# Kernel tuning notes

Hardware: AMD Instinct MI355X
Metric: run time of the kernel (lower is better)

Reference implementation:

```python
import jax, jax.numpy as jnp
import numpy as np

DEPTH = 4
NUM_HEADS = 8
SCALE = 0.25  # (128/8)**-0.5


def _ln(x, g, b):
    m = x.mean(-1, keepdims=True)
    v = ((x - m) ** 2).mean(-1, keepdims=True)
    return (x - m) / jnp.sqrt(v + 1e-5) * g + b


def _mlp_stack(x, params):
    # AsymFormer's MLP default activation is identity, so pure linear stack
    for w, b in params:
        x = x @ w + b
    return x


def _forward(joint_in, relation_in, conn,
             je_w1, je_b1, je_w2, je_b2, je_w3, je_b3,
             re_w1, re_b1, re_w2, re_b2, re_w3, re_b3,
             qkv_w, qkv_b, rconv_w, rconv_b, proj_w, proj_b,
             ln1_g, ln1_b, ln2_g, ln2_b, ln3_g, ln3_b,
             mw1, mb1, mw2, mb2, ng, nb,
             dw1, db1, dw2, db2, dw3, db3):
    jf = _mlp_stack(joint_in, [(je_w1, je_b1), (je_w2, je_b2), (je_w3, je_b3)])
    rf = _mlp_stack(relation_in, [(re_w1, re_b1), (re_w2, re_b2), (re_w3, re_b3)])  # (B,N,N,C)
    B, N, C = jf.shape
    H = NUM_HEADS
    HS = C // H
    for i in range(DEPTH):
        x = _ln(jf, ln1_g[i], ln1_b[i])
        r = _ln(rf, ln2_g[i], ln2_b[i])
        qkv = (x @ qkv_w[i] + qkv_b[i]).reshape(B, N, 3, H, HS)
        q = qkv[:, :, 0].transpose(0, 2, 1, 3)  # (B,H,N,HS)
        k = qkv[:, :, 1].transpose(0, 2, 1, 3)
        v = qkv[:, :, 2].transpose(0, 2, 1, 3)
        attn_J = jnp.einsum('bhnd,bhmd->bhnm', q, k)
        attn_R = (r @ rconv_w[i] + rconv_b[i]).transpose(0, 3, 1, 2)  # (B,H,N,N)
        attn = (attn_J + attn_R) * conn[:, None, :, :] * SCALE
        attn = jax.nn.softmax(attn, axis=-1)
        o = jnp.einsum('bhnm,bhmd->bhnd', attn, v).transpose(0, 2, 1, 3).reshape(B, N, C)
        jf = jf + (o @ proj_w[i] + proj_b[i])
        h = _ln(jf, ln3_g[i], ln3_b[i])
        h = jax.nn.gelu(h @ mw1[i] + mb1[i], approximate=False) @ mw2[i] + mb2[i]
        jf = jf + h
    jf = _ln(jf, ng, nb)
    return _mlp_stack(jf, [(dw1, db1), (dw2, db2), (dw3, db3)])


def setup_inputs() -> dict:
    key = jax.random.key(0)
    ks = iter(jax.random.split(key, 64))
    B, N, C, H, Dp = 8, 256, 128, 8, DEPTH

    def rn(shape, s=0.02):
        return jax.random.normal(next(ks), shape, jnp.float32) * s

    inp = {}
    inp['joint_in'] = jax.random.normal(next(ks), (B, N, 96), jnp.float32)
    inp['relation_in'] = jax.random.normal(next(ks), (B, N, N, 26), jnp.float32)
    inp['conn'] = jax.random.uniform(next(ks), (B, N, N), jnp.float32)
    # joint encoder 96->256->256->128
    for j, (di, do) in enumerate([(96, 256), (256, 256), (256, 128)]):
        inp[f'je_w{j+1}'] = rn((di, do)); inp[f'je_b{j+1}'] = jnp.zeros((do,), jnp.float32)
    # relation encoder 26->256->256->128
    for j, (di, do) in enumerate([(26, 256), (256, 256), (256, 128)]):
        inp[f're_w{j+1}'] = rn((di, do)); inp[f're_b{j+1}'] = jnp.zeros((do,), jnp.float32)
    # per-block params (stacked over depth)
    inp['qkv_w'] = rn((Dp, C, 3 * C)); inp['qkv_b'] = jnp.zeros((Dp, 3 * C), jnp.float32)
    inp['rconv_w'] = rn((Dp, C, H)); inp['rconv_b'] = jnp.zeros((Dp, H), jnp.float32)
    inp['proj_w'] = rn((Dp, C, C)); inp['proj_b'] = jnp.zeros((Dp, C), jnp.float32)
    for nm in ['ln1', 'ln2', 'ln3']:
        inp[f'{nm}_g'] = jnp.ones((Dp, C), jnp.float32)
        inp[f'{nm}_b'] = jnp.zeros((Dp, C), jnp.float32)
    inp['mw1'] = rn((Dp, C, C)); inp['mb1'] = jnp.zeros((Dp, C), jnp.float32)
    inp['mw2'] = rn((Dp, C, C)); inp['mb2'] = jnp.zeros((Dp, C), jnp.float32)
    inp['ng'] = jnp.ones((C,), jnp.float32); inp['nb'] = jnp.zeros((C,), jnp.float32)
    # decoder 128->256->512->90
    for j, (di, do) in enumerate([(128, 256), (256, 512), (512, 90)]):
        inp[f'dw{j+1}'] = rn((di, do)); inp[f'db{j+1}'] = jnp.zeros((do,), jnp.float32)
    return inp


def reference(joint_in, relation_in, conn,
              je_w1, je_b1, je_w2, je_b2, je_w3, je_b3,
              re_w1, re_b1, re_w2, re_b2, re_w3, re_b3,
              qkv_w, qkv_b, rconv_w, rconv_b, proj_w, proj_b,
              ln1_g, ln1_b, ln2_g, ln2_b, ln3_g, ln3_b,
              mw1, mb1, mw2, mb2, ng, nb,
              dw1, db1, dw2, db2, dw3, db3):
    return _forward(joint_in, relation_in, conn,
                    je_w1, je_b1, je_w2, je_b2, je_w3, je_b3,
                    re_w1, re_b1, re_w2, re_b2, re_w3, re_b3,
                    qkv_w, qkv_b, rconv_w, rconv_b, proj_w, proj_b,
                    ln1_g, ln1_b, ln2_g, ln2_b, ln3_g, ln3_b,
                    mw1, mb1, mw2, mb2, ng, nb,
                    dw1, db1, dw2, db2, dw3, db3)
```

## Files before the change

kernel.cpp:

```cpp
#include <hip/hip_runtime.h>
#include <hip/hip_bf16.h>
#include <math.h>

typedef __hip_bfloat16 bf16;
typedef __attribute__((ext_vector_type(8))) short short8;
typedef __attribute__((ext_vector_type(4))) short s16x4;
typedef __attribute__((ext_vector_type(4))) float f32x4;
typedef __attribute__((ext_vector_type(2))) float f32x2;

#define Bb 8
#define Nn 256
#define Hh 8
#define DEPTHd 4
#define BN 2048
#define RTOT 524288
#define RELB 8192
#define JB 32
#define XTS 136
#define X3S 136

__device__ inline float toF(float v) { return v; }
__device__ inline float toF(bf16 v) { return __bfloat162float(v); }
__device__ inline void stF(float* p, float v) { *p = v; }
__device__ inline void stF(bf16* p, float v) { *p = __float2bfloat16(v); }

__global__ __launch_bounds__(256) void k_relF(
    const float* __restrict__ rin, const bf16* __restrict__ W123t,
    const float* __restrict__ b123, const bf16* __restrict__ gWt,
    const float* __restrict__ sgW, const float* __restrict__ bconst,
    bf16* __restrict__ attnR, const float* __restrict__ jin,
    const bf16* __restrict__ Wj123t, const float* __restrict__ bj123,
    float* __restrict__ jf) {
  __shared__ __align__(16) char smem[17920];
  bf16* x3 = (bf16*)smem;
  float* sstatF = (float*)(smem + 17408);

  const int t = threadIdx.x;
  const int lane = t & 63, wv = t >> 6;
  const int lrow = lane & 15, quad = lane >> 4;
  const bool rel = blockIdx.x < RELB;

  if (!rel) {
    const long r0j = (long)(blockIdx.x - RELB) * 64;
    const long gj = r0j + wv * 16 + lrow;
    short8 aj[3];
#pragma unroll
    for (int ks = 0; ks < 3; ++ks) {
      const float* ap = &jin[gj * 96 + ks * 32 + quad * 8];
      f32x4 f0 = *(const f32x4*)ap;
      f32x4 f1 = *(const f32x4*)(ap + 4);
      bf16 pk[8];
#pragma unroll
      for (int u = 0; u < 4; ++u) {
        pk[u] = __float2bfloat16(f0[u]);
        pk[u + 4] = __float2bfloat16(f1[u]);
      }
      aj[ks] = *(short8*)pk;
    }
#pragma unroll
    for (int cb = 0; cb < 4; ++cb)
#pragma unroll
      for (int ct = 0; ct < 2; ++ct) {
        int colb = cb * 32 + ct * 16;
        f32x4 x = {0.f, 0.f, 0.f, 0.f};
#pragma unroll
        for (int ks = 0; ks < 3; ++ks) {
          short8 bw = *(const short8*)&Wj123t[(colb + lrow) * 96 + ks * 32 + quad * 8];
          x = __builtin_amdgcn_mfma_f32_16x16x32_bf16(bw, aj[ks], x, 0, 0, 0);
        }
        f32x4 bq = *(const f32x4*)&bj123[colb + quad * 4];
        f32x4 out;
#pragma unroll
        for (int r = 0; r < 4; ++r) out[r] = x[r] + bq[r];
        *(f32x4*)&jf[gj * 128 + colb + quad * 4] = out;
      }
    return;
  }

  short8 a0;
  {
    const long gr = (long)blockIdx.x * 64 + wv * 16 + lrow;
    const float* ap = &rin[gr * 26];
    float v[8];
    if (quad < 3) {
#pragma unroll
      for (int u = 0; u < 4; ++u) {
        f32x2 f = *(const f32x2*)(ap + quad * 8 + u * 2);
        v[u * 2] = f[0];
        v[u * 2 + 1] = f[1];
      }
    } else {
      f32x2 f = *(const f32x2*)(ap + 24);
      v[0] = f[0];
      v[1] = f[1];
#pragma unroll
      for (int u = 2; u < 8; ++u) v[u] = 0.f;
    }
    bf16 pk[8];
#pragma unroll
    for (int u = 0; u < 8; ++u) pk[u] = __float2bfloat16(v[u]);
    a0 = *(short8*)pk;
  }

  float s1 = 0.f, s2 = 0.f;
#pragma unroll
  for (int cb = 0; cb < 4; ++cb)
#pragma unroll
    for (int ct = 0; ct < 2; ++ct) {
      int colb = cb * 32 + ct * 16;
      f32x4 x = {0.f, 0.f, 0.f, 0.f};
      short8 bw = *(const short8*)&W123t[(colb + lrow) * 32 + quad * 8];
      x = __builtin_amdgcn_mfma_f32_16x16x32_bf16(bw, a0, x, 0, 0, 0);
      f32x4 bq = *(const f32x4*)&b123[colb + quad * 4];
      bf16 pk[4];
#pragma unroll
      for (int r = 0; r < 4; ++r) {
        float v = x[r] + bq[r];
        pk[r] = __float2bfloat16(v);
        s1 += v;
        s2 += v * v;
      }
      *(s16x4*)&x3[(wv * 16 + lrow) * X3S + colb + quad * 4] = *(s16x4*)pk;
    }
  s1 += __shfl_xor(s1, 16, 64);
  s2 += __shfl_xor(s2, 16, 64);
  s1 += __shfl_xor(s1, 32, 64);
  s2 += __shfl_xor(s2, 32, 64);
  if (quad == 0) {
    int row = wv * 16 + lrow;
    float mu = s1 * (1.f / 128.f);
    float var = s2 * (1.f / 128.f) - mu * mu;
    sstatF[row * 2] = mu;
    sstatF[row * 2 + 1] = rsqrtf(var + 1e-5f);
  }
  short8 aw0[4], aw1[4];
#pragma unroll
  for (int kk = 0; kk < 4; ++kk) {
    aw0[kk] = *(const short8*)&gWt[lrow * 128 + kk * 32 + quad * 8];
    aw1[kk] = *(const short8*)&gWt[(16 + lrow) * 128 + kk * 32 + quad * 8];
  }
  __syncthreads();

  {
    f32x4 ac0 = {0.f, 0.f, 0.f, 0.f}, ac1 = {0.f, 0.f, 0.f, 0.f};
#pragma unroll
    for (int kk = 0; kk < 4; ++kk) {
      short8 bbx = *(const short8*)&x3[(wv * 16 + lrow) * X3S + kk * 32 + quad * 8];
      ac0 = __builtin_amdgcn_mfma_f32_16x16x32_bf16(aw0[kk], bbx, ac0, 0, 0, 0);
      ac1 = __builtin_amdgcn_mfma_f32_16x16x32_bf16(aw1[kk], bbx, ac1, 0, 0, 0);
    }
    const long r0 = (long)blockIdx.x * 64;
    int drow = wv * 16 + lrow;
    long gr = r0 + drow;
    float mu = sstatF[drow * 2], inv = sstatF[drow * 2 + 1];
    int bb_ = (int)(gr >> 16);
    int nn = (int)((gr >> 8) & 255);
    int mm = (int)(gr & 255);
#pragma unroll
    for (int mt = 0; mt < 2; ++mt) {
      f32x4 a = mt ? ac1 : ac0;
#pragma unroll
      for (int reg = 0; reg < 4; ++reg) {
        int col = mt * 16 + quad * 4 + reg;
        float v = inv * (a[reg] - mu * sgW[col]) + bconst[col];
        int dd = col >> 3, hh = col & 7;
        attnR[((((long)dd * Bb + bb_) * Hh + hh) * Nn + nn) * Nn + mm] =
            __float2bfloat16(v);
      }
    }
  }
}

__global__ void k_prep0(const float* re_w1, const float* re_w2, const float* re_b1,
                        const float* re_b2, const float* je_w1, const float* je_w2,
                        const float* je_b1, const float* je_b2, const float* dw2,
                        const float* dw3, const float* db1, const float* ln2_g,
                        const float* ln2_b, const float* rconv_w, const float* rconv_b,
                        const float* qkv_w, const float* proj_w, const float* mw1,
                        const float* mw2, float* F, float* bT, float* Fj, float* bTj,
                        float* G, float* u1, bf16* gWt, float* sgW, float* bconst,
                        bf16* Wq, bf16* Wp, bf16* Wm1, bf16* Wm2) {
  const int stride = gridDim.x * blockDim.x;
  const int tid = blockIdx.x * blockDim.x + threadIdx.x;
  for (int i = tid; i < 26 * 256; i += stride) {
    int k = i >> 8, d = i & 255;
    float v = 0.f;
    for (int c = 0; c < 256; ++c) v += re_w1[k * 256 + c] * re_w2[c * 256 + d];
    F[i] = v;
  }
  for (int i = tid; i < 256; i += stride) {
    float v = 0.f;
    for (int c = 0; c < 256; ++c) v += re_b1[c] * re_w2[c * 256 + i];
    bT[i] = v + re_b2[i];
  }
  for (int i = tid; i < 96 * 256; i += stride) {
    int k = i >> 8, d = i & 255;
    float v = 0.f;
    for (int c = 0; c < 256; ++c) v += je_w1[k * 256 + c] * je_w2[c * 256 + d];
    Fj[i] = v;
  }
  for (int i = tid; i < 256; i += stride) {
    float v = 0.f;
    for (int c = 0; c < 256; ++c) v += je_b1[c] * je_w2[c * 256 + i];
    bTj[i] = v + je_b2[i];
  }
  for (int i = tid; i < 256 * 90; i += stride) {
    int c = i / 90, m = i - c * 90;
    float v = 0.f;
    for (int d = 0; d < 512; ++d) v += dw2[c * 512 + d] * dw3[d * 90 + m];
    G[i] = v;
  }
  for (int i = tid; i < 512; i += stride) {
    float v = 0.f;
    for (int c = 0; c < 256; ++c) v += db1[c] * dw2[c * 512 + i];
    u1[i] = v;
  }
  for (int i = tid; i < 32 * 128; i += stride) {
    int col = i >> 7, c = i & 127;
    int dd = col >> 3, h = col & 7;
    gWt[i] = __float2bfloat16(ln2_g[dd * 128 + c] * rconv_w[(dd * 128 + c) * 8 + h]);
  }
  if (tid < 32) {
    int dd = tid >> 3, h = tid & 7;
    float sg = 0.f, bc = 0.f;
    for (int c = 0; c < 128; ++c) {
      float w = rconv_w[(dd * 128 + c) * 8 + h];
      sg += ln2_g[dd * 128 + c] * w;
      bc += ln2_b[dd * 128 + c] * w;
    }
    sgW[tid] = sg;
    bconst[tid] = bc + rconv_b[tid];
  }
  for (int i = tid; i < 4 * 384 * 128; i += stride) {
    int d = i / 49152, rem = i - d * 49152;
    int n = rem >> 7, k = rem & 127;
    Wq[i] = __float2bfloat16(qkv_w[d * 49152 + k * 384 + n]);
  }
  for (int i = tid; i < 4 * 128 * 128; i += stride) {
    int d = i >> 14, rem = i & 16383;
    int n = rem >> 7, k = rem & 127;
    Wp[i] = __float2bfloat16(proj_w[d * 16384 + k * 128 + n]);
    Wm1[i] = __float2bfloat16(mw1[d * 16384 + k * 128 + n]);
    Wm2[i] = __float2bfloat16(mw2[d * 16384 + k * 128 + n]);
  }
}

__global__ void k_prep1(const float* F, const float* bT, const float* re_w3,
                        const float* re_b3, const float* Fj, const float* bTj,
                        const float* je_w3, const float* je_b3, const float* dw1,
                        const float* G, const float* u1, const float* db2,
                        const float* dw3, const float* db3, bf16* W123t, float* b123,
                        bf16* Wj123t, float* bj123, bf16* Wd123t, float* bd123p) {
  const int stride = gridDim.x * blockDim.x;
  const int tid = blockIdx.x * blockDim.x + threadIdx.x;
  for (int i = tid; i < 128 * 32; i += stride) {
    int m = i >> 5, k = i & 31;
    float v = 0.f;
    if (k < 26)
      for (int d = 0; d < 256; ++d) v += F[k * 256 + d] * re_w3[d * 128 + m];
    W123t[i] = __float2bfloat16(v);
  }
  for (int i = tid; i < 128; i += stride) {
    float v = 0.f;
    for (int d = 0; d < 256; ++d) v += bT[d] * re_w3[d * 128 + i];
    b123[i] = v + re_b3[i];
  }
  for (int i = tid; i < 128 * 96; i += stride) {
    int m = i / 96, k = i - m * 96;
    float v = 0.f;
    for (int d = 0; d < 256; ++d) v += Fj[k * 256 + d] * je_w3[d * 128 + m];
    Wj123t[i] = __float2bfloat16(v);
  }
  for (int i = tid; i < 128; i += stride) {
    float v = 0.f;
    for (int d = 0; d < 256; ++d) v += bTj[d] * je_w3[d * 128 + i];
    bj123[i] = v + je_b3[i];
  }
  for (int i = tid; i < 128 * 128; i += stride) {
    int m = i >> 7, k = i & 127;
    float v = 0.f;
    if (m < 90)
      for (int c = 0; c < 256; ++c) v += dw1[k * 256 + c] * G[c * 90 + m];
    Wd123t[i] = __float2bfloat16(v);
  }
  for (int i = tid; i < 128; i += stride) {
    float v = 0.f;
    if (i < 90) {
      for (int d = 0; d < 512; ++d) v += (u1[d] + db2[d]) * dw3[d * 90 + i];
      v += db3[i];
    }
    bd123p[i] = v;
  }
}

template <typename TC>
__global__ __launch_bounds__(256) void k_lnqkv(
    const float* __restrict__ A, const float* __restrict__ g,
    const float* __restrict__ b, const bf16* __restrict__ Bt,
    const float* __restrict__ bias, TC* __restrict__ C, int ldc, int ncols) {
  __shared__ __align__(16) bf16 sX[32 * XTS];
  const int t = threadIdx.x;
  const int lane = t & 63;
  const int wv = t >> 6;
  const int lrow = lane & 15, quad = lane >> 4;
  const long row0 = (long)blockIdx.y * 32;
  const int n0 = blockIdx.x * 128;

  {
    int row = t >> 3, prt = t & 7;
    const float* ap = &A[(row0 + row) * 128 + prt * 16];
    float v[16];
    float s1 = 0.f, s2 = 0.f;
#pragma unroll
    for (int u = 0; u < 4; ++u) {
      f32x4 q = *(const f32x4*)(ap + u * 4);
#pragma unroll
      for (int e = 0; e < 4; ++e) {
        v[u * 4 + e] = q[e];
        s1 += q[e];
        s2 += q[e] * q[e];
      }
    }
    s1 += __shfl_xor(s1, 1, 64);
    s2 += __shfl_xor(s2, 1, 64);
    s1 += __shfl_xor(s1, 2, 64);
    s2 += __shfl_xor(s2, 2, 64);
    s1 += __shfl_xor(s1, 4, 64);
    s2 += __shfl_xor(s2, 4, 64);
    float mu = s1 * (1.f / 128.f);
    float inv = rsqrtf(s2 * (1.f / 128.f) - mu * mu + 1e-5f);
#pragma unroll
    for (int u4 = 0; u4 < 4; ++u4) {
      bf16 pk[4];
#pragma unroll
      for (int e = 0; e < 4; ++e) {
        int c = prt * 16 + u4 * 4 + e;
        pk[e] = __float2bfloat16((v[u4 * 4 + e] - mu) * inv * g[c] + b[c]);
      }
      *(s16x4*)&sX[row * XTS + prt * 16 + u4 * 4] = *(s16x4*)pk;
    }
  }
  __syncthreads();

  f32x4 acc[2][2];
#pragma unroll
  for (int i = 0; i < 2; ++i)
#pragma unroll
    for (int j = 0; j < 2; ++j) {
      f32x4 z = {0.f, 0.f, 0.f, 0.f};
      acc[i][j] = z;
    }
#pragma unroll
  for (int k0 = 0; k0 < 128; k0 += 32) {
    short8 af[2], bfr[2];
#pragma unroll
    for (int j = 0; j < 2; ++j)
      bfr[j] = *(const short8*)&Bt[(long)(n0 + wv * 32 + j * 16 + lrow) * 128 + k0 +
                                   quad * 8];
#pragma unroll
    for (int i = 0; i < 2; ++i)
      af[i] = *(const short8*)&sX[(i * 16 + lrow) * XTS + k0 + quad * 8];
#pragma unroll
    for (int i = 0; i < 2; ++i)
#pragma unroll
      for (int j = 0; j < 2; ++j)
        acc[i][j] =
            __builtin_amdgcn_mfma_f32_16x16x32_bf16(af[i], bfr[j], acc[i][j], 0, 0, 0);
  }
#pragma unroll
  for (int i = 0; i < 2; ++i) {
#pragma unroll
    for (int r = 0; r < 4; ++r) {
      long gr = row0 + i * 16 + quad * 4 + r;
#pragma unroll
      for (int j = 0; j < 2; ++j) {
        int gc = n0 + wv * 32 + j * 16 + lrow;
        if (gc < ncols) stF(&C[gr * (long)ldc + gc], acc[i][j][r] + bias[gc]);
      }
    }
  }
}

template <bool QKV>
__global__ __launch_bounds__(256) void k_tailq(
    const bf16* __restrict__ obuf, float* __restrict__ jf, const bf16* __restrict__ Wp,
    const float* __restrict__ pb, const float* __restrict__ g3,
    const float* __restrict__ b3, const bf16* __restrict__ Wm1,
    const float* __restrict__ m1b, const bf16* __restrict__ Wm2,
    const float* __restrict__ m2b, const float* __restrict__ g1n,
    const float* __restrict__ b1n, const bf16* __restrict__ Wqn,
    const float* __restrict__ qbn, float* __restrict__ qkvb) {
  __shared__ __align__(16) bf16 sX[16 * XTS];
  __shared__ __align__(16) bf16 sH[16 * XTS];
  __shared__ float sstat[16][4][2];
  __shared__ float sstatF[16][2];

  const int t = threadIdx.x;
  const int lane = t & 63;
  const int wv = t >> 6;
  const int lrow = lane & 15, quad = lane >> 4;
  const long row0 = (long)blockIdx.x * 16;

  {
    int r = t >> 4, c8 = (t & 15) * 8;
    *(uint4*)&sX[r * XTS + c8] = *(const uint4*)&obuf[(row0 + r) * 128 + c8];
  }
  __syncthreads();

  f32x4 acc[2];
  {
    f32x4 z = {0.f, 0.f, 0.f, 0.f};
    acc[0] = z;
    acc[1] = z;
  }
#pragma unroll
  for (int k0 = 0; k0 < 128; k0 += 32) {
    short8 af = *(const short8*)&sX[lrow * XTS + k0 + quad * 8];
    short8 bfr[2];
#pragma unroll
    for (int j = 0; j < 2; ++j)
      bfr[j] = *(const short8*)&Wp[(wv * 32 + j * 16 + lrow) * 128 + k0 + quad * 8];
#pragma unroll
    for (int j = 0; j < 2; ++j)
      acc[j] = __builtin_amdgcn_mfma_f32_16x16x32_bf16(af, bfr[j], acc[j], 0, 0, 0);
  }
#pragma unroll
  for (int r = 0; r < 4; ++r) {
    int rl = quad * 4 + r;
    long gr = row0 + rl;
    float s1 = 0.f, s2 = 0.f;
#pragma unroll
    for (int j = 0; j < 2; ++j) {
      int gc = wv * 32 + j * 16 + lrow;
      float v = acc[j][r] + pb[gc] + jf[gr * 128 + gc];
      acc[j][r] = v;
      jf[gr * 128 + gc] = v;
      s1 += v;
      s2 += v * v;
    }
#pragma unroll
    for (int m = 1; m < 16; m <<= 1) {
      s1 += __shfl_xor(s1, m, 64);
      s2 += __shfl_xor(s2, m, 64);
    }
    if (lrow == 0) {
      sstat[rl][wv][0] = s1;
      sstat[rl][wv][1] = s2;
    }
  }
  __syncthreads();
  if (t < 16) {
    float s1 = 0.f, s2 = 0.f;
#pragma unroll
    for (int w = 0; w < 4; ++w) {
      s1 += sstat[t][w][0];
      s2 += sstat[t][w][1];
    }
    float mu = s1 * (1.f / 128.f);
    float var = s2 * (1.f / 128.f) - mu * mu;
    sstatF[t][0] = mu;
    sstatF[t][1] = rsqrtf(var + 1e-5f);
  }
  __syncthreads();
#pragma unroll
  for (int r = 0; r < 4; ++r) {
    int rl = quad * 4 + r;
    float mu = sstatF[rl][0], inv = sstatF[rl][1];
#pragma unroll
    for (int j = 0; j < 2; ++j) {
      int gc = wv * 32 + j * 16 + lrow;
      sX[rl * XTS + gc] = __float2bfloat16((acc[j][r] - mu) * inv * g3[gc] + b3[gc]);
    }
  }
  __syncthreads();

  f32x4 acc2[2];
  {
    f32x4 z = {0.f, 0.f, 0.f, 0.f};
    acc2[0] = z;
    acc2[1] = z;
  }
#pragma unroll
  for (int k0 = 0; k0 < 128; k0 += 32) {
    short8 af = *(const short8*)&sX[lrow * XTS + k0 + quad * 8];
    short8 bfr[2];
#pragma unroll
    for (int j = 0; j < 2; ++j)
      bfr[j] = *(const short8*)&Wm1[(wv * 32 + j * 16 + lrow) * 128 + k0 + quad * 8];
#pragma unroll
    for (int j = 0; j < 2; ++j)
      acc2[j] = __builtin_amdgcn_mfma_f32_16x16x32_bf16(af, bfr[j], acc2[j], 0, 0, 0);
  }
#pragma unroll
  for (int r = 0; r < 4; ++r) {
    int rl = quad * 4 + r;
#pragma unroll
    for (int j = 0; j < 2; ++j) {
      int gc = wv * 32 + j * 16 + lrow;
      float v = acc2[j][r] + m1b[gc];
      v = 0.5f * v * (1.f + erff(v * 0.70710678118654752f));
      sH[rl * XTS + gc] = __float2bfloat16(v);
    }
  }
  __syncthreads();

  f32x4 acc3[2];
  {
    f32x4 z = {0.f, 0.f, 0.f, 0.f};
    acc3[0] = z;
    acc3[1] = z;
  }
#pragma unroll
  for (int k0 = 0; k0 < 128; k0 += 32) {
    short8 af = *(const short8*)&sH[lrow * XTS + k0 + quad * 8];
    short8 bfr[2];
#pragma unroll
    for (int j = 0; j < 2; ++j)
      bfr[j] = *(const short8*)&Wm2[(wv * 32 + j * 16 + lrow) * 128 + k0 + quad * 8];
#pragma unroll
    for (int j = 0; j < 2; ++j)
      acc3[j] = __builtin_amdgcn_mfma_f32_16x16x32_bf16(af, bfr[j], acc3[j], 0, 0, 0);
  }
#pragma unroll
  for (int r = 0; r < 4; ++r) {
    int rl = quad * 4 + r;
    long gr = row0 + rl;
    float s1 = 0.f, s2 = 0.f;
#pragma unroll
    for (int j = 0; j < 2; ++j) {
      int gc = wv * 32 + j * 16 + lrow;
      float v = acc3[j][r] + m2b[gc] + jf[gr * 128 + gc];
      acc3[j][r] = v;
      jf[gr * 128 + gc] = v;
      if (QKV) {
        s1 += v;
        s2 += v * v;
      }
    }
    if (QKV) {
#pragma unroll
      for (int m = 1; m < 16; m <<= 1) {
        s1 += __shfl_xor(s1, m, 64);
        s2 += __shfl_xor(s2, m, 64);
      }
      if (lrow == 0) {
        sstat[rl][wv][0] = s1;
        sstat[rl][wv][1] = s2;
      }
    }
  }
  if (!QKV) return;
  __syncthreads();
  if (t < 16) {
    float s1 = 0.f, s2 = 0.f;
#pragma unroll
    for (int w = 0; w < 4; ++w) {
      s1 += sstat[t][w][0];
      s2 += sstat[t][w][1];
    }
    float mu = s1 * (1.f / 128.f);
    float var = s2 * (1.f / 128.f) - mu * mu;
    sstatF[t][0] = mu;
    sstatF[t][1] = rsqrtf(var + 1e-5f);
  }
  __syncthreads();
#pragma unroll
  for (int r = 0; r < 4; ++r) {
    int rl = quad * 4 + r;
    float mu = sstatF[rl][0], inv = sstatF[rl][1];
#pragma unroll
    for (int j = 0; j < 2; ++j) {
      int gc = wv * 32 + j * 16 + lrow;
      sX[rl * XTS + gc] = __float2bfloat16((acc3[j][r] - mu) * inv * g1n[gc] + b1n[gc]);
    }
  }
  __syncthreads();
  for (int p = 0; p < 3; ++p) {
    f32x4 acc4[2];
    {
      f32x4 z = {0.f, 0.f, 0.f, 0.f};
      acc4[0] = z;
      acc4[1] = z;
    }
#pragma unroll
    for (int k0 = 0; k0 < 128; k0 += 32) {
      short8 af = *(const short8*)&sX[lrow * XTS + k0 + quad * 8];
      short8 bfr[2];
#pragma unroll
      for (int j = 0; j < 2; ++j)
        bfr[j] = *(const short8*)&Wqn[(long)(p * 128 + wv * 32 + j * 16 + lrow) * 128 +
                                      k0 + quad * 8];
#pragma unroll
      for (int j = 0; j < 2; ++j)
        acc4[j] = __builtin_amdgcn_mfma_f32_16x16x32_bf16(af, bfr[j], acc4[j], 0, 0, 0);
    }
#pragma unroll
    for (int r = 0; r < 4; ++r) {
      long gr = row0 + quad * 4 + r;
#pragma unroll
      for (int j = 0; j < 2; ++j) {
        int gc = p * 128 + wv * 32 + j * 16 + lrow;
        qkvb[gr * 384 + gc] = acc4[j][r] + qbn[gc];
      }
    }
  }
}

__global__ __launch_bounds__(256) void k_attn(const float* __restrict__ qkv,
                                              const bf16* __restrict__ aR,
                                              const float* __restrict__ conn,
                                              bf16* __restrict__ obuf) {
  __shared__ float p[4][4 * 68];
  const int wv = threadIdx.x >> 6;
  const int n = blockIdx.x * 4 + wv;
  const int h = blockIdx.y, b = blockIdx.z;
  const int lane = threadIdx.x & 63;
  const long rowq = (long)(b * Nn + n);
  const float* qp = &qkv[rowq * 384 + h * 16];
  f32x4 q0 = *(const f32x4*)qp;
  f32x4 q1 = *(const f32x4*)(qp + 4);
  f32x4 q2 = *(const f32x4*)(qp + 8);
  f32x4 q3 = *(const f32x4*)(qp + 12);
  const bf16* arp = &aR[((long)(b * Hh + h) * Nn + n) * Nn];
  const float* cnp = &conn[rowq * Nn];

  float lg[4];
#pragma unroll
  for (int s = 0; s < 4; ++s) {
    int m = s * 64 + lane;
    const float* kp = &qkv[((long)(b * Nn + m)) * 384 + 128 + h * 16];
    f32x4 k0 = *(const f32x4*)kp;
    f32x4 k1 = *(const f32x4*)(kp + 4);
    f32x4 k2 = *(const f32x4*)(kp + 8);
    f32x4 k3 = *(const f32x4*)(kp + 12);
    float d = 0.f;
#pragma unroll
    for (int e = 0; e < 4; ++e)
      d += q0[e] * k0[e] + q1[e] * k1[e] + q2[e] * k2[e] + q3[e] * k3[e];
    d += __bfloat162float(arp[m]);
    lg[s] = d * cnp[m] * 0.25f;
  }
  float mx = fmaxf(fmaxf(lg[0], lg[1]), fmaxf(lg[2], lg[3]));
#pragma unroll
  for (int off = 32; off; off >>= 1) mx = fmaxf(mx, __shfl_xor(mx, off, 64));
  float ex[4], ssum = 0.f;
#pragma unroll
  for (int s = 0; s < 4; ++s) {
    ex[s] = expf(lg[s] - mx);
    ssum += ex[s];
  }
#pragma unroll
  for (int off = 32; off; off >>= 1) ssum += __shfl_xor(ssum, off, 64);
#pragma unroll
  for (int s = 0; s < 4; ++s) p[wv][s * 68 + lane] = ex[s];
  float rinv = 1.f / ssum;

  const int c = lane & 15, sg = lane >> 4;
  const float* vp = &qkv[((long)(b * Nn + sg * 64)) * 384 + 256 + h * 16 + c];
  float acc = 0.f;
#pragma unroll
  for (int u = 0; u < 16; ++u) {
    f32x4 pq = *(const f32x4*)&p[wv][sg * 68 + u * 4];
#pragma unroll
    for (int e = 0; e < 4; ++e) acc += pq[e] * vp[(long)(u * 4 + e) * 384];
  }
  acc += __shfl_xor(acc, 16, 64);
  acc += __shfl_xor(acc, 32, 64);
  if (lane < 16) obuf[rowq * 128 + h * 16 + lane] = __float2bfloat16(acc * rinv);
}

extern "C" void kernel_launch(void* const* d_in, const int* in_sizes, int n_in,
                              void* d_out, int out_size, void* d_ws, size_t ws_size,
                              hipStream_t stream) {
  const float* joint_in = (const float*)d_in[0];
  const float* relation_in = (const float*)d_in[1];
  const float* conn = (const float*)d_in[2];
  const float* je_w1 = (const float*)d_in[3];
  const float* je_b1 = (const float*)d_in[4];
  const float* je_w2 = (const float*)d_in[5];
  const float* je_b2 = (const float*)d_in[6];
  const float* je_w3 = (const float*)d_in[7];
  const float* je_b3 = (const float*)d_in[8];
  const float* re_w1 = (const float*)d_in[9];
  const float* re_b1 = (const float*)d_in[10];
  const float* re_w2 = (const float*)d_in[11];
  const float* re_b2 = (const float*)d_in[12];
  const float* re_w3 = (const float*)d_in[13];
  const float* re_b3 = (const float*)d_in[14];
  const float* qkv_w = (const float*)d_in[15];
  const float* qkv_b = (const float*)d_in[16];
  const float* rconv_w = (const float*)d_in[17];
  const float* rconv_b = (const float*)d_in[18];
  const float* proj_w = (const float*)d_in[19];
  const float* proj_b = (const float*)d_in[20];
  const float* ln1_g = (const float*)d_in[21];
  const float* ln1_b = (const float*)d_in[22];
  const float* ln2_g = (const float*)d_in[23];
  const float* ln2_b = (const float*)d_in[24];
  const float* ln3_g = (const float*)d_in[25];
  const float* ln3_b = (const float*)d_in[26];
  const float* mw1 = (const float*)d_in[27];
  const float* mb1 = (const float*)d_in[28];
  const float* mw2 = (const float*)d_in[29];
  const float* mb2 = (const float*)d_in[30];
  const float* ng = (const float*)d_in[31];
  const float* nb = (const float*)d_in[32];
  const float* dw1 = (const float*)d_in[33];
  const float* db1 = (const float*)d_in[34];
  const float* dw2 = (const float*)d_in[35];
  const float* db2 = (const float*)d_in[36];
  const float* dw3 = (const float*)d_in[37];
  const float* db3 = (const float*)d_in[38];

  char* ws = (char*)d_ws;
  size_t off = 0;
  auto alloc = [&](size_t bytes) -> void* {
    void* p = ws + off;
    off += (bytes + 255) & ~(size_t)255;
    return p;
  };
  bf16* attnR = (bf16*)alloc((size_t)DEPTHd * Bb * Hh * Nn * Nn * 2);
  bf16* gWt = (bf16*)alloc(32 * 128 * 2);
  float* sgW = (float*)alloc(32 * 4);
  float* bconst = (float*)alloc(32 * 4);
  bf16* Wq = (bf16*)alloc(4 * 384 * 128 * 2);
  bf16* Wp = (bf16*)alloc(4 * 128 * 128 * 2);
  bf16* Wm1 = (bf16*)alloc(4 * 128 * 128 * 2);
  bf16* Wm2 = (bf16*)alloc(4 * 128 * 128 * 2);
  bf16* W123t = (bf16*)alloc(128 * 32 * 2);
  float* b123 = (float*)alloc(128 * 4);
  bf16* Wj123t = (bf16*)alloc(128 * 96 * 2);
  float* bj123 = (float*)alloc(128 * 4);
  bf16* Wd123t = (bf16*)alloc(128 * 128 * 2);
  float* bd123p = (float*)alloc(128 * 4);
  float* F = (float*)alloc(26 * 256 * 4);
  float* bT = (float*)alloc(256 * 4);
  float* Fj = (float*)alloc(96 * 256 * 4);
  float* bTj = (float*)alloc(256 * 4);
  float* G = (float*)alloc(256 * 90 * 4);
  float* u1 = (float*)alloc(512 * 4);
  float* jf = (float*)alloc((size_t)BN * 128 * 4);
  bf16* obuf = (bf16*)alloc((size_t)BN * 128 * 2);
  char* U = (char*)alloc((size_t)BN * 384 * 4);
  float* qkvb = (float*)U;

  k_prep0<<<dim3(256), dim3(256), 0, stream>>>(
      re_w1, re_w2, re_b1, re_b2, je_w1, je_w2, je_b1, je_b2, dw2, dw3, db1,
      ln2_g, ln2_b, rconv_w, rconv_b, qkv_w, proj_w, mw1, mw2,
      F, bT, Fj, bTj, G, u1, gWt, sgW, bconst, Wq, Wp, Wm1, Wm2);
  k_prep1<<<dim3(64), dim3(256), 0, stream>>>(
      F, bT, re_w3, re_b3, Fj, bTj, je_w3, je_b3, dw1, G, u1, db2, dw3, db3,
      W123t, b123, Wj123t, bj123, Wd123t, bd123p);

  k_relF<<<dim3(RELB + JB), dim3(256), 0, stream>>>(
      relation_in, W123t, b123, gWt, sgW, bconst, attnR, joint_in, Wj123t, bj123, jf);

  k_lnqkv<float><<<dim3(3, 64), dim3(256), 0, stream>>>(
      jf, ln1_g, ln1_b, Wq, qkv_b, qkvb, 384, 384);

  for (int d = 0; d < DEPTHd; ++d) {
    k_attn<<<dim3(Nn / 4, Hh, Bb), dim3(256), 0, stream>>>(
        qkvb, attnR + (size_t)d * Bb * Hh * Nn * Nn, conn, obuf);
    if (d < 3) {
      k_tailq<true><<<dim3(128), dim3(256), 0, stream>>>(
          obuf, jf, Wp + (size_t)d * 16384, proj_b + d * 128, ln3_g + d * 128,
          ln3_b + d * 128, Wm1 + (size_t)d * 16384, mb1 + d * 128,
          Wm2 + (size_t)d * 16384, mb2 + d * 128, ln1_g + (d + 1) * 128,
          ln1_b + (d + 1) * 128, Wq + (size_t)(d + 1) * 49152, qkv_b + (d + 1) * 384,
          qkvb);
    } else {
      k_tailq<false><<<dim3(128), dim3(256), 0, stream>>>(
          obuf, jf, Wp + (size_t)d * 16384, proj_b + d * 128, ln3_g + d * 128,
          ln3_b + d * 128, Wm1 + (size_t)d * 16384, mb1 + d * 128,
          Wm2 + (size_t)d * 16384, mb2 + d * 128, nullptr, nullptr, nullptr, nullptr,
          nullptr);
    }
  }

  k_lnqkv<float><<<dim3(1, 64), dim3(256), 0, stream>>>(
      jf, ng, nb, Wd123t, bd123p, (float*)d_out, 90, 90);
}
```

Baseline: 613.5 us.

## Spread weight-folding prep across more blocks and fold weight casts into relF

The two prep kernels previously ran grid-stride loops over a small grid, with each thread serially looping over long dot products for several phases in sequence. They now assign each phase its own block range (one block per output row), so all phases run concurrently across many more blocks. The bf16 transposed weight conversion for the qkv, proj and MLP layers moves out of prep into extra blocks appended to the relation-feature kernel, where it overlaps with the large relation work. This shortens the serial prep at the head of the pipeline, at the cost of more launched blocks and a larger relF grid.

```diff
diff --git a/kernel.cpp b/kernel.cpp
--- a/kernel.cpp
+++ b/kernel.cpp
@@ -16,6 +16,7 @@
 #define RTOT 524288
 #define RELB 8192
 #define JB 32
+#define PREPB 64
 #define XTS 136
 #define X3S 136
 
@@ -30,12 +31,35 @@
     const float* __restrict__ sgW, const float* __restrict__ bconst,
     bf16* __restrict__ attnR, const float* __restrict__ jin,
     const bf16* __restrict__ Wj123t, const float* __restrict__ bj123,
-    float* __restrict__ jf) {
+    float* __restrict__ jf,
+    const float* __restrict__ qkv_w, const float* __restrict__ proj_w,
+    const float* __restrict__ mw1, const float* __restrict__ mw2,
+    bf16* __restrict__ Wq, bf16* __restrict__ Wp, bf16* __restrict__ Wm1,
+    bf16* __restrict__ Wm2) {
+  const int t = threadIdx.x;
+
+  if (blockIdx.x >= RELB + JB) {
+    const int stride = PREPB * 256;
+    const int tid = (blockIdx.x - (RELB + JB)) * 256 + t;
+    for (int i = tid; i < 4 * 384 * 128; i += stride) {
+      int d = i / 49152, rem = i - d * 49152;
+      int n = rem >> 7, k = rem & 127;
+      Wq[i] = __float2bfloat16(qkv_w[d * 49152 + k * 384 + n]);
+    }
+    for (int i = tid; i < 4 * 128 * 128; i += stride) {
+      int d = i >> 14, rem = i & 16383;
+      int n = rem >> 7, k = rem & 127;
+      Wp[i] = __float2bfloat16(proj_w[d * 16384 + k * 128 + n]);
+      Wm1[i] = __float2bfloat16(mw1[d * 16384 + k * 128 + n]);
+      Wm2[i] = __float2bfloat16(mw2[d * 16384 + k * 128 + n]);
+    }
+    return;
+  }
+
   __shared__ __align__(16) char smem[17920];
   bf16* x3 = (bf16*)smem;
   float* sstatF = (float*)(smem + 17408);
 
-  const int t = threadIdx.x;
   const int lane = t & 63, wv = t >> 6;
   const int lrow = lane & 15, quad = lane >> 4;
   const bool rel = blockIdx.x < RELB;
@@ -171,125 +195,118 @@
   }
 }
 
-__global__ void k_prep0(const float* re_w1, const float* re_w2, const float* re_b1,
-                        const float* re_b2, const float* je_w1, const float* je_w2,
-                        const float* je_b1, const float* je_b2, const float* dw2,
-                        const float* dw3, const float* db1, const float* ln2_g,
-                        const float* ln2_b, const float* rconv_w, const float* rconv_b,
-                        const float* qkv_w, const float* proj_w, const float* mw1,
-                        const float* mw2, float* F, float* bT, float* Fj, float* bTj,
-                        float* G, float* u1, bf16* gWt, float* sgW, float* bconst,
-                        bf16* Wq, bf16* Wp, bf16* Wm1, bf16* Wm2) {
-  const int stride = gridDim.x * blockDim.x;
-  const int tid = blockIdx.x * blockDim.x + threadIdx.x;
-  for (int i = tid; i < 26 * 256; i += stride) {
-    int k = i >> 8, d = i & 255;
+__global__ __launch_bounds__(256) void k_prepA(
+    const float* re_w1, const float* re_w2, const float* re_b1, const float* re_b2,
+    const float* je_w1, const float* je_w2, const float* je_b1, const float* je_b2,
+    const float* dw2, const float* dw3, const float* db1, const float* ln2_g,
+    const float* ln2_b, const float* rconv_w, const float* rconv_b, float* F,
+    float* bT, float* Fj, float* bTj, float* G, float* u1, bf16* gWt, float* sgW,
+    float* bconst) {
+  const int b = blockIdx.x, t = threadIdx.x;
+  if (b < 26) {
+    int k = b, d = t;
     float v = 0.f;
     for (int c = 0; c < 256; ++c) v += re_w1[k * 256 + c] * re_w2[c * 256 + d];
-    F[i] = v;
-  }
-  for (int i = tid; i < 256; i += stride) {
+    F[k * 256 + d] = v;
+  } else if (b == 26) {
+    int d = t;
     float v = 0.f;
-    for (int c = 0; c < 256; ++c) v += re_b1[c] * re_w2[c * 256 + i];
-    bT[i] = v + re_b2[i];
-  }
-  for (int i = tid; i < 96 * 256; i += stride) {
-    int k = i >> 8, d = i & 255;
+    for (int c = 0; c < 256; ++c) v += re_b1[c] * re_w2[c * 256 + d];
+    bT[d] = v + re_b2[d];
+  } else if (b < 123) {
+    int k = b - 27, d = t;
     float v = 0.f;
     for (int c = 0; c < 256; ++c) v += je_w1[k * 256 + c] * je_w2[c * 256 + d];
-    Fj[i] = v;
-  }
-  for (int i = tid; i < 256; i += stride) {
+    Fj[k * 256 + d] = v;
+  } else if (b == 123) {
+    int d = t;
     float v = 0.f;
-    for (int c = 0; c < 256; ++c) v += je_b1[c] * je_w2[c * 256 + i];
-    bTj[i] = v + je_b2[i];
-  }
-  for (int i = tid; i < 256 * 90; i += stride) {
-    int c = i / 90, m = i - c * 90;
-    float v = 0.f;
-    for (int d = 0; d < 512; ++d) v += dw2[c * 512 + d] * dw3[d * 90 + m];
-    G[i] = v;
-  }
-  for (int i = tid; i < 512; i += stride) {
-    float v = 0.f;
-    for (int c = 0; c < 256; ++c) v += db1[c] * dw2[c * 512 + i];
-    u1[i] = v;
-  }
-  for (int i = tid; i < 32 * 128; i += stride) {
+    for (int c = 0; c < 256; ++c) v += je_b1[c] * je_w2[c * 256 + d];
+    bTj[d] = v + je_b2[d];
+  } else if (b < 380) {
+    int c = b - 124, m = t;
+    if (m < 90) {
+      float v = 0.f;
+      for (int d = 0; d < 512; ++d) v += dw2[c * 512 + d] * dw3[d * 90 + m];
+      G[c * 90 + m] = v;
+    }
+  } else if (b == 380) {
+    for (int i = t; i < 512; i += 256) {
+      float v = 0.f;
+      for (int c = 0; c < 256; ++c) v += db1[c] * dw2[c * 512 + i];
+      u1[i] = v;
+    }
+  } else if (b < 397) {
+    int i = (b - 381) * 256 + t;
     int col = i >> 7, c = i & 127;
     int dd = col >> 3, h = col & 7;
     gWt[i] = __float2bfloat16(ln2_g[dd * 128 + c] * rconv_w[(dd * 128 + c) * 8 + h]);
-  }
-  if (tid < 32) {
-    int dd = tid >> 3, h = tid & 7;
-    float sg = 0.f, bc = 0.f;
-    for (int c = 0; c < 128; ++c) {
-      float w = rconv_w[(dd * 128 + c) * 8 + h];
-      sg += ln2_g[dd * 128 + c] * w;
-      bc += ln2_b[dd * 128 + c] * w;
-    }
-    sgW[tid] = sg;
-    bconst[tid] = bc + rconv_b[tid];
-  }
-  for (int i = tid; i < 4 * 384 * 128; i += stride) {
-    int d = i / 49152, rem = i - d * 49152;
-    int n = rem >> 7, k = rem & 127;
-    Wq[i] = __float2bfloat16(qkv_w[d * 49152 + k * 384 + n]);
-  }
-  for (int i = tid; i < 4 * 128 * 128; i += stride) {
-    int d = i >> 14, rem = i & 16383;
-    int n = rem >> 7, k = rem & 127;
-    Wp[i] = __float2bfloat16(proj_w[d * 16384 + k * 128 + n]);
-    Wm1[i] = __float2bfloat16(mw1[d * 16384 + k * 128 + n]);
-    Wm2[i] = __float2bfloat16(mw2[d * 16384 + k * 128 + n]);
+  } else {
+    if (t < 32) {
+      int dd = t >> 3, h = t & 7;
+      float sg = 0.f, bc = 0.f;
+      for (int c = 0; c < 128; ++c) {
+        float w = rconv_w[(dd * 128 + c) * 8 + h];
+        sg += ln2_g[dd * 128 + c] * w;
+        bc += ln2_b[dd * 128 + c] * w;
+      }
+      sgW[t] = sg;
+      bconst[t] = bc + rconv_b[t];
+    }
   }
 }
 
-__global__ void k_prep1(const float* F, const float* bT, const float* re_w3,
-                        const float* re_b3, const float* Fj, const float* bTj,
-                        const float* je_w3, const float* je_b3, const float* dw1,
-                        const float* G, const float* u1, const float* db2,
-                        const float* dw3, const float* db3, bf16* W123t, float* b123,
-                        bf16* Wj123t, float* bj123, bf16* Wd123t, float* bd123p) {
-  const int stride = gridDim.x * blockDim.x;
-  const int tid = blockIdx.x * blockDim.x + threadIdx.x;
-  for (int i = tid; i < 128 * 32; i += stride) {
-    int m = i >> 5, k = i & 31;
-    float v = 0.f;
-    if (k < 26)
-      for (int d = 0; d < 256; ++d) v += F[k * 256 + d] * re_w3[d * 128 + m];
-    W123t[i] = __float2bfloat16(v);
-  }
-  for (int i = tid; i < 128; i += stride) {
-    float v = 0.f;
-    for (int d = 0; d < 256; ++d) v += bT[d] * re_w3[d * 128 + i];
-    b123[i] = v + re_b3[i];
-  }
-  for (int i = tid; i < 128 * 96; i += stride) {
-    int m = i / 96, k = i - m * 96;
-    float v = 0.f;
-    for (int d = 0; d < 256; ++d) v += Fj[k * 256 + d] * je_w3[d * 128 + m];
-    Wj123t[i] = __float2bfloat16(v);
-  }
-  for (int i = tid; i < 128; i += stride) {
-    float v = 0.f;
-    for (int d = 0; d < 256; ++d) v += bTj[d] * je_w3[d * 128 + i];
-    bj123[i] = v + je_b3[i];
-  }
-  for (int i = tid; i < 128 * 128; i += stride) {
-    int m = i >> 7, k = i & 127;
-    float v = 0.f;
-    if (m < 90)
-      for (int c = 0; c < 256; ++c) v += dw1[k * 256 + c] * G[c * 90 + m];
-    Wd123t[i] = __float2bfloat16(v);
-  }
-  for (int i = tid; i < 128; i += stride) {
-    float v = 0.f;
-    if (i < 90) {
-      for (int d = 0; d < 512; ++d) v += (u1[d] + db2[d]) * dw3[d * 90 + i];
-      v += db3[i];
-    }
-    bd123p[i] = v;
+__global__ __launch_bounds__(256) void k_prepB(
+    const float* F, const float* bT, const float* re_w3, const float* re_b3,
+    const float* Fj, const float* bTj, const float* je_w3, const float* je_b3,
+    const float* dw1, const float* G, const float* u1, const float* db2,
+    const float* dw3, const float* db3, bf16* W123t, float* b123, bf16* Wj123t,
+    float* bj123, bf16* Wd123t, float* bd123p) {
+  const int b = blockIdx.x, t = threadIdx.x;
+  if (b < 32) {
+    if (t < 128) {
+      int k = b, m = t;
+      float v = 0.f;
+      if (k < 26)
+        for (int d = 0; d < 256; ++d) v += F[k * 256 + d] * re_w3[d * 128 + m];
+      W123t[m * 32 + k] = __float2bfloat16(v);
+    }
+  } else if (b == 32) {
+    if (t < 128) {
+      float v = 0.f;
+      for (int d = 0; d < 256; ++d) v += bT[d] * re_w3[d * 128 + t];
+      b123[t] = v + re_b3[t];
+    }
+  } else if (b < 129) {
+    if (t < 128) {
+      int k = b - 33, m = t;
+      float v = 0.f;
+      for (int d = 0; d < 256; ++d) v += Fj[k * 256 + d] * je_w3[d * 128 + m];
+      Wj123t[m * 96 + k] = __float2bfloat16(v);
+    }
+  } else if (b == 129) {
+    if (t < 128) {
+      float v = 0.f;
+      for (int d = 0; d < 256; ++d) v += bTj[d] * je_w3[d * 128 + t];
+      bj123[t] = v + je_b3[t];
+    }
+  } else if (b < 258) {
+    if (t < 128) {
+      int k = b - 130, m = t;
+      float v = 0.f;
+      if (m < 90)
+        for (int c = 0; c < 256; ++c) v += dw1[k * 256 + c] * G[c * 90 + m];
+      Wd123t[m * 128 + k] = __float2bfloat16(v);
+    }
+  } else {
+    if (t < 128) {
+      float v = 0.f;
+      if (t < 90) {
+        for (int d = 0; d < 512; ++d) v += (u1[d] + db2[d]) * dw3[d * 90 + t];
+        v += db3[t];
+      }
+      bd123p[t] = v;
+    }
   }
 }
 
@@ -744,16 +761,16 @@
   char* U = (char*)alloc((size_t)BN * 384 * 4);
   float* qkvb = (float*)U;
 
-  k_prep0<<<dim3(256), dim3(256), 0, stream>>>(
+  k_prepA<<<dim3(398), dim3(256), 0, stream>>>(
       re_w1, re_w2, re_b1, re_b2, je_w1, je_w2, je_b1, je_b2, dw2, dw3, db1,
-      ln2_g, ln2_b, rconv_w, rconv_b, qkv_w, proj_w, mw1, mw2,
-      F, bT, Fj, bTj, G, u1, gWt, sgW, bconst, Wq, Wp, Wm1, Wm2);
-  k_prep1<<<dim3(64), dim3(256), 0, stream>>>(
+      ln2_g, ln2_b, rconv_w, rconv_b, F, bT, Fj, bTj, G, u1, gWt, sgW, bconst);
+  k_prepB<<<dim3(259), dim3(256), 0, stream>>>(
       F, bT, re_w3, re_b3, Fj, bTj, je_w3, je_b3, dw1, G, u1, db2, dw3, db3,
       W123t, b123, Wj123t, bj123, Wd123t, bd123p);
 
-  k_relF<<<dim3(RELB + JB), dim3(256), 0, stream>>>(
-      relation_in, W123t, b123, gWt, sgW, bconst, attnR, joint_in, Wj123t, bj123, jf);
+  k_relF<<<dim3(RELB + JB + PREPB), dim3(256), 0, stream>>>(
+      relation_in, W123t, b123, gWt, sgW, bconst, attnR, joint_in, Wj123t, bj123, jf,
+      qkv_w, proj_w, mw1, mw2, Wq, Wp, Wm1, Wm2);
 
   k_lnqkv<float><<<dim3(3, 64), dim3(256), 0, stream>>>(
       jf, ln1_g, ln1_b, Wq, qkv_b, qkvb, 384, 384);
```

Result: faster. 526.8 us (-14.1%).
